# Optimization experiments

Measured on AMD Instinct MI355X. Metric: run time of the kernel, lower is better.

The kernel has to match this reference:

```python
import jax, jax.numpy as jnp
import numpy as np

B, T, NV, DEG, E = 64, 256, 20000, 8, 128
NSEG, NBUCKET = NV * DEG, 288
F_DIST, F_DIR, F_TT, HID = 50, 50, 50, 100
FEED = 2 * E + F_DIST + F_DIR  # 356


def setup_inputs() -> dict:
    key = jax.random.key(0)
    ks = jax.random.split(key, 32)
    s = 1.0 / np.sqrt(E)
    return {
        "xs_padded": jax.random.randint(ks[0], (B, T), 0, NV),
        "lengths": jax.random.randint(ks[1], (B,), 8, T + 1),
        "xs_actions": jax.random.randint(ks[2], (B, T - 1), 0, DEG),
        "destinations": jax.random.randint(ks[3], (B,), 0, NV),
        "adj_list": jax.random.randint(ks[4], (NV, DEG), 0, NV),
        "seg_ids": jax.random.randint(ks[5], (NV, DEG), 0, NSEG),
        "start_time": 42,
        "locations": jax.random.normal(ks[6], (NV, 2)),
        "time_dist_seg": jax.random.uniform(ks[7], (NSEG, NBUCKET)) * 10.0,
        "emb": jax.random.normal(ks[8], (NV + 2, E)) * 0.01,
        "Wq": jax.random.normal(ks[9], (E, E)) * s,
        "Wk": jax.random.normal(ks[10], (E, E)) * s,
        "Wv": jax.random.normal(ks[11], (E, E)) * s,
        "Wo": jax.random.normal(ks[12], (E, E)) * s,
        "dist_W": jax.random.normal(ks[13], (1, F_DIST)),
        "dist_b": jnp.zeros((F_DIST,)),
        "dir_W": jax.random.normal(ks[14], (2, F_DIR)) * 0.7,
        "dir_b": jnp.zeros((F_DIR,)),
        "tt_W": jax.random.normal(ks[15], (1, F_TT)),
        "tt_b": jnp.zeros((F_TT,)),
        "ob_W1": jax.random.normal(ks[16], (F_TT, F_TT // 2)) * (1.0 / np.sqrt(F_TT)),
        "ob_b1": jnp.zeros((F_TT // 2,)),
        "ob_W2": jax.random.normal(ks[17], (F_TT // 2, 1)) * (1.0 / np.sqrt(F_TT // 2)),
        "ob_b2": jnp.zeros((1,)),
        "om_W1": jax.random.normal(ks[18], (FEED, HID)) * (1.0 / np.sqrt(FEED)),
        "om_b1": jnp.zeros((HID,)),
        "om_W2": jax.random.normal(ks[19], (HID, HID // 2)) * (1.0 / np.sqrt(HID)),
        "om_b2": jnp.zeros((HID // 2,)),
        "om_W3": jax.random.normal(ks[20], (HID // 2, 1)) * (1.0 / np.sqrt(HID // 2)),
        "om_b3": jnp.zeros((1,)),
    }


def reference(xs_padded, lengths, xs_actions, destinations, adj_list, seg_ids,
              start_time, locations, time_dist_seg, emb, Wq, Wk, Wv, Wo,
              dist_W, dist_b, dir_W, dir_b, tt_W, tt_b,
              ob_W1, ob_b1, ob_W2, ob_b2,
              om_W1, om_b1, om_W2, om_b2, om_W3, om_b3):
    # --- embeddings + causal/padding-masked self-attention (flash_att) ---
    x_e = emb[xs_padded]                                       # [B,T,E]
    q, k, v = x_e @ Wq, x_e @ Wk, x_e @ Wv
    scores = jnp.einsum('bqe,bke->bqk', q, k) / jnp.sqrt(jnp.float32(E))
    causal = jnp.triu(jnp.ones((T, T), bool), 1)
    pad = jnp.arange(T)[None, :] >= lengths[:, None]           # key padding [B,T]
    scores = jnp.where(causal[None] | pad[:, None, :], -1e9, scores)
    hidden = jnp.einsum('bqk,bke->bqe', jax.nn.softmax(scores, axis=-1), v) @ Wo

    # --- irregular neighbor gather: route_neighbors only filled for t < len-1 ---
    valid_t = jnp.arange(T)[None, :] < (lengths - 1)[:, None]  # [B,T]
    rn = jnp.where(valid_t[:, :, None], adj_list[xs_padded], 0)  # [B,T,DEG]

    # --- distance to destination feature ---
    dest_c = locations[destinations][:, None, None, :]         # [B,1,1,2]
    nbr_c = locations[rn]                                      # [B,T,DEG,2]
    dist = jnp.abs(nbr_c - dest_c).sum(-1, keepdims=True) * 100.0
    dist_f = dist @ dist_W + dist_b

    # --- direction (unit vector) feature ---
    vec = nbr_c - locations[xs_padded][:, :, None, :]
    unit = vec / (jnp.linalg.norm(vec, axis=-1, keepdims=True) + 1e-8)
    dir_f = unit @ dir_W + dir_b

    # --- travel-time lookup + masked whitening ---
    nmask = rn != 0
    tt = time_dist_seg[seg_ids[xs_padded], start_time]         # [B,T,DEG]
    mf = nmask.astype(tt.dtype)
    cnt = mf.sum()
    mean = (tt * mf).sum() / cnt
    var = (((tt - mean) ** 2) * mf).sum() / (cnt - 1.0)        # unbiased, like torch.std
    tt = (tt - mean) / (jnp.sqrt(var) + 1e-6)
    tt_f = (tt[..., None] @ tt_W + tt_b) * mf[..., None]

    # --- fuse and score neighbors ---
    hid_e = jnp.broadcast_to(hidden[:, :, None, :], (B, T, DEG, E))
    dest_e = jnp.broadcast_to(emb[destinations][:, None, None, :], (B, T, DEG, E))
    feed = jnp.concatenate([hid_e, dist_f, dir_f, dest_e], axis=-1)  # [B,T,DEG,356]

    ob = (jax.nn.relu(tt_f @ ob_W1 + ob_b1) @ ob_W2 + ob_b2).squeeze(-1)
    h1 = jax.nn.relu(feed @ om_W1 + om_b1)
    h2 = jax.nn.relu(h1 @ om_W2 + om_b2)
    logits = (h2 @ om_W3 + om_b3).squeeze(-1) + ob             # [B,T,DEG]

    # --- per-route mean cross-entropy over valid transitions, summed over batch ---
    logp = jax.nn.log_softmax(logits[:, :T - 1], axis=-1)
    nll = -jnp.take_along_axis(logp, xs_actions[..., None], axis=-1).squeeze(-1)
    vmask = (jnp.arange(T - 1)[None, :] < (lengths - 1)[:, None]).astype(nll.dtype)
    per = (nll * vmask).sum(1) / (lengths - 1).astype(nll.dtype)
    return per.sum()
```

## Files before the change

### kernel.cpp

```cpp
#include <hip/hip_runtime.h>
#include <math.h>

#define BB 64
#define TT 256
#define DEG 8
#define EE 128
#define NBUCKET 288
#define HID 100
#define H2 50

constexpr size_t OFF_STATS   = 0;
constexpr size_t OFF_CDIST   = 4;
constexpr size_t OFF_CDIRX   = 104;
constexpr size_t OFF_CDIRY   = 204;
constexpr size_t OFF_BASE    = 304;
constexpr size_t OFF_V25     = 404;
constexpr size_t OFF_C25     = 429;
constexpr size_t OFF_OBZ     = 454;
constexpr size_t OFF_DESTPRE = 456;
constexpr size_t OFF_WF      = 6856;
constexpr size_t OFF_TT      = 32456;
constexpr size_t OFF_Q       = 163528;
constexpr size_t OFF_K       = OFF_Q + 16384 * 128;
constexpr size_t OFF_VP      = OFF_K + 16384 * 128;
constexpr size_t OFF_H1P     = OFF_VP + 16384 * 100;

__global__ void __launch_bounds__(256) k_setup(
    const int* destinations, const float* emb, const float* Wo,
    const float* dist_W, const float* dist_b, const float* dir_W, const float* dir_b,
    const float* tt_W, const float* tt_b, const float* ob_W1, const float* ob_b1,
    const float* ob_W2, const float* ob_b2, const float* om_W1, const float* om_b1,
    float* ws, float* out) {
    __shared__ float sh[EE];
    int blk = blockIdx.x;
    int j = threadIdx.x;
    if (blk == 0) {
        if (j < 4) ws[OFF_STATS + j] = 0.f;
        if (j == 0) out[0] = 0.f;
        if (j < HID) {
            float cd = 0.f, cx = 0.f, cy = 0.f, bs = om_b1[j];
            for (int f = 0; f < 50; f++) {
                float w1d = om_W1[(128 + f) * HID + j];
                float w1r = om_W1[(178 + f) * HID + j];
                cd += dist_W[f] * w1d;
                bs += dist_b[f] * w1d + dir_b[f] * w1r;
                cx += dir_W[f] * w1r;
                cy += dir_W[50 + f] * w1r;
            }
            ws[OFF_CDIST + j] = cd; ws[OFF_CDIRX + j] = cx;
            ws[OFF_CDIRY + j] = cy; ws[OFF_BASE + j] = bs;
        }
        if (j >= 128 && j < 153) {
            int jj = j - 128;
            float v = 0.f, c = ob_b1[jj];
            for (int i = 0; i < 50; i++) {
                v += tt_W[i] * ob_W1[i * 25 + jj];
                c += tt_b[i] * ob_W1[i * 25 + jj];
            }
            ws[OFF_V25 + jj] = v; ws[OFF_C25 + jj] = c;
        }
        if (j == 200) {
            float z = ob_b2[0];
            for (int i = 0; i < 25; i++) z += fmaxf(ob_b1[i], 0.f) * ob_W2[i];
            ws[OFF_OBZ] = z;
        }
    } else if (blk <= 64) {
        int b = blk - 1;
        if (j < EE) sh[j] = emb[(size_t)destinations[b] * EE + j];
        __syncthreads();
        if (j < HID) {
            float acc = 0.f;
            for (int i = 0; i < EE; i++) acc += sh[i] * om_W1[(228 + i) * HID + j];
            ws[OFF_DESTPRE + b * HID + j] = acc;
        }
    } else {
        int i = blk - 65;
        if (j < EE) sh[j] = Wo[i * EE + j];
        __syncthreads();
        if (j < HID) {
            float acc = 0.f;
            for (int jj = 0; jj < EE; jj++) acc += sh[jj] * om_W1[jj * HID + j];
            ws[OFF_WF + i * HID + j] = acc;
        }
    }
}

__global__ void __launch_bounds__(256) k_mid(
    const int* xs, const int* lengths, const int* adj, const int* seg,
    const int* stime, const float* tds, const float* emb,
    const float* Wq, const float* Wk, const float* Wv, float* ws) {
    __shared__ float smem[2 * 128 * 36 + 32];
    int blk = blockIdx.x;
    int tid = threadIdx.x;
    if (blk < 512) {
        float (*XT)[36]  = (float(*)[36])smem;
        float (*T1T)[36] = (float(*)[36])(smem + 128 * 36);
        int* vids = (int*)(smem + 2 * 128 * 36);
        int r0 = blk * 32;
        if (tid < 32) vids[tid] = xs[r0 + tid];
        __syncthreads();
        for (int c = 0; c < 16; c++) {
            int idx = c * 256 + tid;
            int r = idx >> 7, i = idx & 127;
            XT[i][r] = emb[(size_t)vids[r] * EE + i];
        }
        __syncthreads();
        int cg = tid & 31, rg = tid >> 5;
        const float* Wmats[2] = {Wq, Wk};
        float* Omats[2] = {ws + OFF_Q, ws + OFF_K};
        for (int mtx = 0; mtx < 2; mtx++) {
            const float* W = Wmats[mtx];
            float acc[4][4];
            #pragma unroll
            for (int a = 0; a < 4; a++)
                #pragma unroll
                for (int bb = 0; bb < 4; bb++) acc[a][bb] = 0.f;
            #pragma unroll 4
            for (int i = 0; i < EE; i++) {
                float4 av = *(const float4*)&XT[i][rg << 2];
                float4 wv = *(const float4*)&W[i * EE + (cg << 2)];
                acc[0][0] += av.x * wv.x; acc[0][1] += av.x * wv.y; acc[0][2] += av.x * wv.z; acc[0][3] += av.x * wv.w;
                acc[1][0] += av.y * wv.x; acc[1][1] += av.y * wv.y; acc[1][2] += av.y * wv.z; acc[1][3] += av.y * wv.w;
                acc[2][0] += av.z * wv.x; acc[2][1] += av.z * wv.y; acc[2][2] += av.z * wv.z; acc[2][3] += av.z * wv.w;
                acc[3][0] += av.w * wv.x; acc[3][1] += av.w * wv.y; acc[3][2] += av.w * wv.z; acc[3][3] += av.w * wv.w;
            }
            float* O = Omats[mtx];
            #pragma unroll
            for (int jj = 0; jj < 4; jj++)
                *(float4*)&O[(size_t)(r0 + (rg << 2) + jj) * EE + (cg << 2)] =
                    make_float4(acc[jj][0], acc[jj][1], acc[jj][2], acc[jj][3]);
        }
        {
            float acc[4][4];
            #pragma unroll
            for (int a = 0; a < 4; a++)
                #pragma unroll
                for (int bb = 0; bb < 4; bb++) acc[a][bb] = 0.f;
            #pragma unroll 4
            for (int i = 0; i < EE; i++) {
                float4 av = *(const float4*)&XT[i][rg << 2];
                float4 wv = *(const float4*)&Wv[i * EE + (cg << 2)];
                acc[0][0] += av.x * wv.x; acc[0][1] += av.x * wv.y; acc[0][2] += av.x * wv.z; acc[0][3] += av.x * wv.w;
                acc[1][0] += av.y * wv.x; acc[1][1] += av.y * wv.y; acc[1][2] += av.y * wv.z; acc[1][3] += av.y * wv.w;
                acc[2][0] += av.z * wv.x; acc[2][1] += av.z * wv.y; acc[2][2] += av.z * wv.z; acc[2][3] += av.z * wv.w;
                acc[3][0] += av.w * wv.x; acc[3][1] += av.w * wv.y; acc[3][2] += av.w * wv.z; acc[3][3] += av.w * wv.w;
            }
            #pragma unroll
            for (int jj = 0; jj < 4; jj++)
                #pragma unroll
                for (int ii = 0; ii < 4; ii++)
                    T1T[(cg << 2) + ii][(rg << 2) + jj] = acc[jj][ii];
        }
        __syncthreads();
        if (cg < 25) {
            const float* WF = ws + OFF_WF;
            float acc[4][4];
            #pragma unroll
            for (int a = 0; a < 4; a++)
                #pragma unroll
                for (int bb = 0; bb < 4; bb++) acc[a][bb] = 0.f;
            #pragma unroll 4
            for (int i = 0; i < EE; i++) {
                float4 av = *(const float4*)&T1T[i][rg << 2];
                float4 wv = *(const float4*)&WF[i * HID + (cg << 2)];
                acc[0][0] += av.x * wv.x; acc[0][1] += av.x * wv.y; acc[0][2] += av.x * wv.z; acc[0][3] += av.x * wv.w;
                acc[1][0] += av.y * wv.x; acc[1][1] += av.y * wv.y; acc[1][2] += av.y * wv.z; acc[1][3] += av.y * wv.w;
                acc[2][0] += av.z * wv.x; acc[2][1] += av.z * wv.y; acc[2][2] += av.z * wv.z; acc[2][3] += av.z * wv.w;
                acc[3][0] += av.w * wv.x; acc[3][1] += av.w * wv.y; acc[3][2] += av.w * wv.z; acc[3][3] += av.w * wv.w;
            }
            float* VP = ws + OFF_VP;
            #pragma unroll
            for (int jj = 0; jj < 4; jj++)
                *(float4*)&VP[(size_t)(r0 + (rg << 2) + jj) * HID + (cg << 2)] =
                    make_float4(acc[jj][0], acc[jj][1], acc[jj][2], acc[jj][3]);
        }
    } else {
        float* rs = smem; float* rq = smem + 256; float* rc = smem + 512;
        int st = *stime;
        float lsum = 0.f, lsq = 0.f, lcnt = 0.f;
        int total = BB * TT * DEG;
        for (int idx = (blk - 512) * 256 + tid; idx < total; idx += 256 * 256) {
            int d = idx & 7;
            int bt = idx >> 3;
            int t = bt & 255;
            int b = bt >> 8;
            int len = lengths[b];
            if (t >= len - 1) continue;
            int v = xs[bt];
            int sg = seg[v * DEG + d];
            float tt = tds[(size_t)sg * NBUCKET + st];
            ws[OFF_TT + idx] = tt;
            int a = adj[v * DEG + d];
            if (a != 0) { lsum += tt; lsq += tt * tt; lcnt += 1.f; }
        }
        rs[tid] = lsum; rq[tid] = lsq; rc[tid] = lcnt;
        __syncthreads();
        for (int s = 128; s > 0; s >>= 1) {
            if (tid < s) { rs[tid] += rs[tid + s]; rq[tid] += rq[tid + s]; rc[tid] += rc[tid + s]; }
            __syncthreads();
        }
        if (tid == 0) {
            atomicAdd(&ws[OFF_STATS + 0], rs[0]);
            atomicAdd(&ws[OFF_STATS + 1], rq[0]);
            atomicAdd(&ws[OFF_STATS + 2], rc[0]);
        }
    }
}

__global__ void __launch_bounds__(256) k_attn(const int* lengths, float* ws) {
    int b = blockIdx.x >> 4;
    int tile = blockIdx.x & 15;
    int t0 = tile << 4;
    int len = lengths[b];
    if (t0 >= len - 1) return;
    int nk = t0 + 16;
    int nm = nk >> 4;
    __shared__ float Qs[16][132];
    __shared__ float S[16][260];
    __shared__ float KV[32 * 136];
    int tid = threadIdx.x;
    const float* Q  = ws + OFF_Q;
    const float* K  = ws + OFF_K;
    const float* VP = ws + OFF_VP;
    {
        const float* Qg = Q + ((size_t)(b * TT + t0)) * EE;
        for (int idx = tid; idx < 512; idx += 256) {
            int r = idx >> 5, c4 = (idx & 31) << 2;
            *(float4*)&Qs[r][c4] = *(const float4*)&Qg[r * EE + c4];
        }
    }
    int q = tid >> 4, li = tid & 15;
    int tq = t0 + q;
    float sreg[16];
    #pragma unroll
    for (int m = 0; m < 16; m++) sreg[m] = -1e30f;
    float (*Ks)[136] = (float(*)[136])KV;
    int ktend = ((nk + 31) >> 5) << 5;
    for (int kt = 0; kt < ktend; kt += 32) {
        __syncthreads();
        const float* Kg = K + ((size_t)(b * TT + kt)) * EE;
        for (int idx = tid; idx < 1024; idx += 256) {
            int r = idx >> 5, c4 = (idx & 31) << 2;
            *(float4*)&Ks[r][c4] = *(const float4*)&Kg[r * EE + c4];
        }
        __syncthreads();
        int k0 = kt + li, k1 = kt + li + 16;
        float s0 = 0.f, s1 = 0.f;
        const float4* q4  = (const float4*)Qs[q];
        const float4* k4a = (const float4*)Ks[li];
        const float4* k4b = (const float4*)Ks[li + 16];
        #pragma unroll 8
        for (int i = 0; i < 32; i++) {
            float4 a = q4[i];
            float4 x = k4a[i];
            float4 y = k4b[i];
            s0 += a.x * x.x + a.y * x.y + a.z * x.z + a.w * x.w;
            s1 += a.x * y.x + a.y * y.y + a.z * y.z + a.w * y.w;
        }
        int m0 = kt >> 4;
        if (k0 < nk && k0 <= tq) sreg[m0]     = s0 * 0.08838834764831845f;
        if (k1 < nk && k1 <= tq) sreg[m0 + 1] = s1 * 0.08838834764831845f;
    }
    float mx = -1e30f;
    for (int m = 0; m < nm; m++) mx = fmaxf(mx, sreg[m]);
    #pragma unroll
    for (int o = 1; o < 16; o <<= 1) mx = fmaxf(mx, __shfl_xor(mx, o, 16));
    float lsum = 0.f;
    for (int m = 0; m < nm; m++) { float p = __expf(sreg[m] - mx); sreg[m] = p; lsum += p; }
    #pragma unroll
    for (int o = 1; o < 16; o <<= 1) lsum += __shfl_xor(lsum, o, 16);
    float inv = 1.f / lsum;
    for (int m = 0; m < nm; m++) S[q][li + (m << 4)] = sreg[m];
    float acc[7];
    #pragma unroll
    for (int j = 0; j < 7; j++) acc[j] = 0.f;
    float (*Vs)[104] = (float(*)[104])KV;
    for (int vt = 0; vt < nk; vt += 32) {
        __syncthreads();
        const float* Vg = VP + ((size_t)(b * TT + vt)) * HID;
        for (int idx = tid; idx < 800; idx += 256) {
            int r = idx / 25, c4 = (idx - r * 25) << 2;
            *(float4*)&Vs[r][c4] = *(const float4*)&Vg[r * HID + c4];
        }
        __syncthreads();
        int kmax = nk - vt; if (kmax > 32) kmax = 32;
        for (int k = 0; k < kmax; k++) {
            float p = S[q][vt + k];
            #pragma unroll
            for (int j = 0; j < 7; j++) {
                int c = li + (j << 4);
                if (c < HID) acc[j] += p * Vs[k][c];
            }
        }
    }
    if (tq < len - 1) {
        float* H = ws + OFF_H1P + (size_t)(b * TT + tq) * HID;
        const float* BASEv = ws + OFF_BASE;
        const float* DP = ws + OFF_DESTPRE + b * HID;
        #pragma unroll
        for (int j = 0; j < 7; j++) {
            int c = li + (j << 4);
            if (c < HID) H[c] = acc[j] * inv + BASEv[c] + DP[c];
        }
    }
}

__global__ void __launch_bounds__(256) k_final(
    const int* xs, const int* lengths, const int* xs_actions, const int* destinations,
    const int* adj, const float* locations,
    const float* om_W2, const float* om_b2, const float* om_W3, const float* om_b3,
    const float* ob_W2, const float* ob_b2,
    const float* ws, float* out)
{
    __shared__ float W2T[H2][104];
    __shared__ float h1s[4][DEG][104];
    __shared__ float nlls[4];
    int tid = threadIdx.x;
    for (int idx = tid; idx < HID * H2; idx += 256) {
        int mm = idx / H2, n = idx - mm * H2;
        W2T[n][mm] = om_W2[idx];
    }
    if (tid < 4) nlls[tid] = 0.f;
    int w = tid >> 6, lane = tid & 63;
    int r = lane >> 3, li = lane & 7;
    float sum = ws[OFF_STATS], sq = ws[OFF_STATS + 1], cnt = ws[OFF_STATS + 2];
    float mean = sum / cnt;
    float var = (sq - cnt * mean * mean) / (cnt - 1.f);
    float sdinv = 1.f / (sqrtf(var) + 1e-6f);
    __syncthreads();
    for (int it = 0; it < 4; it++) {
        int pi = blockIdx.x * 16 + it * 4 + w;
        int b = pi / (TT - 1), t = pi - b * (TT - 1);
        int len = lengths[b];
        bool valid = (t < len - 1);
        int bt = b * TT + t;
        if (valid) {
            float distv = 0.f, uxv = 0.f, uyv = 0.f, obv = 0.f;
            if (lane < 8) {
                int v = xs[bt];
                int a = adj[v * DEG + lane];
                float nbx = locations[2 * a], nby = locations[2 * a + 1];
                int dst = destinations[b];
                float dxl = locations[2 * dst], dyl = locations[2 * dst + 1];
                float cxl = locations[2 * v], cyl = locations[2 * v + 1];
                distv = (fabsf(nbx - dxl) + fabsf(nby - dyl)) * 100.f;
                float vx = nbx - cxl, vy = nby - cyl;
                float nrm = sqrtf(vx * vx + vy * vy) + 1e-8f;
                uxv = vx / nrm; uyv = vy / nrm;
                float ttn = (ws[OFF_TT + (size_t)bt * 8 + lane] - mean) * sdinv;
                float obp = 0.f;
                for (int j = 0; j < 25; j++)
                    obp += fmaxf(ttn * ws[OFF_V25 + j] + ws[OFF_C25 + j], 0.f) * ob_W2[j];
                obv = (a != 0) ? (obp + ob_b2[0]) : ws[OFF_OBZ];
            }
            distv = __shfl(distv, r, 64);
            uxv   = __shfl(uxv, r, 64);
            uyv   = __shfl(uyv, r, 64);
            obv   = __shfl(obv, r, 64);
            const float* H = ws + OFF_H1P + (size_t)bt * HID;
            for (int mm = li; mm < HID; mm += 8) {
                float pre = H[mm] + distv * ws[OFF_CDIST + mm]
                          + uxv * ws[OFF_CDIRX + mm] + uyv * ws[OFF_CDIRY + mm];
                h1s[w][r][mm] = fmaxf(pre, 0.f);
            }
            float acc[7] = {0.f, 0.f, 0.f, 0.f, 0.f, 0.f, 0.f};
            const float4* hv4 = (const float4*)h1s[w][r];
            for (int ks = 0; ks < 25; ks++) {
                float4 h = hv4[ks];
                #pragma unroll
                for (int j = 0; j < 7; j++) {
                    int n = li + 8 * j;
                    if (n < H2) {
                        float4 wv = *(const float4*)&W2T[n][ks << 2];
                        acc[j] += h.x * wv.x + h.y * wv.y + h.z * wv.z + h.w * wv.w;
                    }
                }
            }
            float part = 0.f;
            #pragma unroll
            for (int j = 0; j < 7; j++) {
                int n = li + 8 * j;
                if (n < H2) part += fmaxf(acc[j] + om_b2[n], 0.f) * om_W3[n];
            }
            part += __shfl_xor(part, 1, 8);
            part += __shfl_xor(part, 2, 8);
            part += __shfl_xor(part, 4, 8);
            float logit = part + om_b3[0] + obv;
            float lgv[8];
            float mx = -1e30f;
            #pragma unroll
            for (int d = 0; d < 8; d++) {
                lgv[d] = __shfl(logit, d << 3, 64);
                mx = fmaxf(mx, lgv[d]);
            }
            if (lane == 0) {
                int act = xs_actions[b * (TT - 1) + t];
                float se = 0.f, sel = 0.f;
                #pragma unroll
                for (int d = 0; d < 8; d++) {
                    se += __expf(lgv[d] - mx);
                    if (d == act) sel = lgv[d];
                }
                float nll = mx + __logf(se) - sel;
                nlls[w] += nll / (float)(len - 1);
            }
        }
    }
    __syncthreads();
    if (tid == 0) {
        atomicAdd(out, nlls[0] + nlls[1] + nlls[2] + nlls[3]);
    }
}

extern "C" void kernel_launch(void* const* d_in, const int* in_sizes, int n_in,
                              void* d_out, int out_size, void* d_ws, size_t ws_size,
                              hipStream_t stream) {
    const int* xs_padded    = (const int*)d_in[0];
    const int* lengths      = (const int*)d_in[1];
    const int* xs_actions   = (const int*)d_in[2];
    const int* destinations = (const int*)d_in[3];
    const int* adj_list     = (const int*)d_in[4];
    const int* seg_ids      = (const int*)d_in[5];
    const int* start_time   = (const int*)d_in[6];
    const float* locations  = (const float*)d_in[7];
    const float* tds        = (const float*)d_in[8];
    const float* emb        = (const float*)d_in[9];
    const float* Wq         = (const float*)d_in[10];
    const float* Wk         = (const float*)d_in[11];
    const float* Wv         = (const float*)d_in[12];
    const float* Wo         = (const float*)d_in[13];
    const float* dist_W     = (const float*)d_in[14];
    const float* dist_b     = (const float*)d_in[15];
    const float* dir_W      = (const float*)d_in[16];
    const float* dir_b      = (const float*)d_in[17];
    const float* tt_W       = (const float*)d_in[18];
    const float* tt_b       = (const float*)d_in[19];
    const float* ob_W1      = (const float*)d_in[20];
    const float* ob_b1      = (const float*)d_in[21];
    const float* ob_W2      = (const float*)d_in[22];
    const float* ob_b2      = (const float*)d_in[23];
    const float* om_W1      = (const float*)d_in[24];
    const float* om_b1      = (const float*)d_in[25];
    const float* om_W2      = (const float*)d_in[26];
    const float* om_b2      = (const float*)d_in[27];
    const float* om_W3      = (const float*)d_in[28];
    const float* om_b3      = (const float*)d_in[29];
    float* ws  = (float*)d_ws;
    float* out = (float*)d_out;

    k_setup<<<193, 256, 0, stream>>>(destinations, emb, Wo, dist_W, dist_b,
                                     dir_W, dir_b, tt_W, tt_b, ob_W1, ob_b1,
                                     ob_W2, ob_b2, om_W1, om_b1, ws, out);
    k_mid<<<768, 256, 0, stream>>>(xs_padded, lengths, adj_list, seg_ids,
                                   start_time, tds, emb, Wq, Wk, Wv, ws);
    k_attn<<<BB * 16, 256, 0, stream>>>(lengths, ws);
    k_final<<<1020, 256, 0, stream>>>(
        xs_padded, lengths, xs_actions, destinations, adj_list, locations,
        om_W2, om_b2, om_W3, om_b3, ob_W2, ob_b2, ws, out);
}
```

Before: 483.9 us.

## Fuse attention and final MLP scoring into one kernel via shared memory

Merges the attention kernel and the final scoring kernel so the per-position hidden pre-activation stays in shared memory rather than being written to and read back from a global workspace buffer. The second MLP layer is reorganised as a register-tiled 2x8 outer-product over a transposed h1 tile, computing all 8 neighbors for 8 queries per pass. This removes one launch and a global round trip, but it adds shared-memory reuse across phases and puts the MLP work on the attention blocks' schedule and occupancy.

Result: faster. 471.5 us (-2.6%).

```diff
diff --git a/kernel.cpp b/kernel.cpp
--- a/kernel.cpp
+++ b/kernel.cpp
@@ -23,7 +23,6 @@
 constexpr size_t OFF_Q       = 163528;
 constexpr size_t OFF_K       = OFF_Q + 16384 * 128;
 constexpr size_t OFF_VP      = OFF_K + 16384 * 128;
-constexpr size_t OFF_H1P     = OFF_VP + 16384 * 100;
 
 __global__ void __launch_bounds__(256) k_setup(
     const int* destinations, const float* emb, const float* Wo,
@@ -207,18 +206,26 @@
     }
 }
 
-__global__ void __launch_bounds__(256) k_attn(const int* lengths, float* ws) {
+__global__ void __launch_bounds__(256) k_attnfinal(
+    const int* lengths, const int* xs, const int* xs_actions,
+    const int* destinations, const int* adj, const float* locations,
+    const float* om_W2, const float* om_b2, const float* om_W3, const float* om_b3,
+    const float* ob_W2, const float* ob_b2,
+    float* ws, float* out) {
     int b = blockIdx.x >> 4;
     int tile = blockIdx.x & 15;
     int t0 = tile << 4;
     int len = lengths[b];
     if (t0 >= len - 1) return;
+    int nqv = len - 1 - t0; if (nqv > 16) nqv = 16;
     int nk = t0 + 16;
     int nm = nk >> 4;
-    __shared__ float Qs[16][132];
-    __shared__ float S[16][260];
-    __shared__ float KV[32 * 136];
+    __shared__ float smem[17696];
+    float (*S)[260]  = (float(*)[260])smem;
+    float (*Qs)[132] = (float(*)[132])(smem + 4160);
+    float* KV = smem + 6272;
     int tid = threadIdx.x;
+    if (tid < 16) smem[17680 + tid] = 0.f;
     const float* Q  = ws + OFF_Q;
     const float* K  = ws + OFF_K;
     const float* VP = ws + OFF_VP;
@@ -293,122 +300,152 @@
             }
         }
     }
-    if (tq < len - 1) {
-        float* H = ws + OFF_H1P + (size_t)(b * TT + tq) * HID;
+    __syncthreads();
+    {
         const float* BASEv = ws + OFF_BASE;
         const float* DP = ws + OFF_DESTPRE + b * HID;
         #pragma unroll
         for (int j = 0; j < 7; j++) {
             int c = li + (j << 4);
-            if (c < HID) H[c] = acc[j] * inv + BASEv[c] + DP[c];
-        }
-    }
-}
-
-__global__ void __launch_bounds__(256) k_final(
-    const int* xs, const int* lengths, const int* xs_actions, const int* destinations,
-    const int* adj, const float* locations,
-    const float* om_W2, const float* om_b2, const float* om_W3, const float* om_b3,
-    const float* ob_W2, const float* ob_b2,
-    const float* ws, float* out)
-{
-    __shared__ float W2T[H2][104];
-    __shared__ float h1s[4][DEG][104];
-    __shared__ float nlls[4];
-    int tid = threadIdx.x;
-    for (int idx = tid; idx < HID * H2; idx += 256) {
-        int mm = idx / H2, n = idx - mm * H2;
-        W2T[n][mm] = om_W2[idx];
-    }
-    if (tid < 4) nlls[tid] = 0.f;
-    int w = tid >> 6, lane = tid & 63;
-    int r = lane >> 3, li = lane & 7;
-    float sum = ws[OFF_STATS], sq = ws[OFF_STATS + 1], cnt = ws[OFF_STATS + 2];
-    float mean = sum / cnt;
-    float var = (sq - cnt * mean * mean) / (cnt - 1.f);
-    float sdinv = 1.f / (sqrtf(var) + 1e-6f);
+            if (c < HID) S[q][c] = acc[j] * inv + BASEv[c] + DP[c];
+        }
+    }
+    float (*W2s)[64] = (float(*)[64])(smem + 4160);
+    for (int idx = tid; idx < 6400; idx += 256) {
+        int mm = idx >> 6, n = idx & 63;
+        W2s[mm][n] = (n < H2) ? om_W2[mm * H2 + n] : 0.f;
+    }
+    float smean, sdinv;
+    {
+        float sum = ws[OFF_STATS], sq = ws[OFF_STATS + 1], cnt = ws[OFF_STATS + 2];
+        smean = sum / cnt;
+        float var = (sq - cnt * smean * smean) / (cnt - 1.f);
+        sdinv = 1.f / (sqrtf(var) + 1e-6f);
+    }
+    float (*h1T)[68] = (float(*)[68])(smem + 10560);
+    float* distR = smem + 17360;
+    float* uxR   = smem + 17424;
+    float* uyR   = smem + 17488;
+    float* obR   = smem + 17552;
+    float* lgS   = smem + 17616;
+    float* nllS  = smem + 17680;
+    int cg = tid & 7, rg = tid >> 3;
+    float b2v[8], w3v[8];
+    #pragma unroll
+    for (int k = 0; k < 8; k++) {
+        int n = (cg << 3) + k;
+        b2v[k] = (n < H2) ? om_b2[n] : 0.f;
+        w3v[k] = (n < H2) ? om_W3[n] : 0.f;
+    }
+    float ob2s = ob_b2[0];
+    float obz = ws[OFF_OBZ];
     __syncthreads();
-    for (int it = 0; it < 4; it++) {
-        int pi = blockIdx.x * 16 + it * 4 + w;
-        int b = pi / (TT - 1), t = pi - b * (TT - 1);
-        int len = lengths[b];
-        bool valid = (t < len - 1);
-        int bt = b * TT + t;
-        if (valid) {
-            float distv = 0.f, uxv = 0.f, uyv = 0.f, obv = 0.f;
-            if (lane < 8) {
-                int v = xs[bt];
-                int a = adj[v * DEG + lane];
-                float nbx = locations[2 * a], nby = locations[2 * a + 1];
-                int dst = destinations[b];
-                float dxl = locations[2 * dst], dyl = locations[2 * dst + 1];
-                float cxl = locations[2 * v], cyl = locations[2 * v + 1];
-                distv = (fabsf(nbx - dxl) + fabsf(nby - dyl)) * 100.f;
-                float vx = nbx - cxl, vy = nby - cyl;
-                float nrm = sqrtf(vx * vx + vy * vy) + 1e-8f;
-                uxv = vx / nrm; uyv = vy / nrm;
-                float ttn = (ws[OFF_TT + (size_t)bt * 8 + lane] - mean) * sdinv;
-                float obp = 0.f;
-                for (int j = 0; j < 25; j++)
-                    obp += fmaxf(ttn * ws[OFF_V25 + j] + ws[OFF_C25 + j], 0.f) * ob_W2[j];
-                obv = (a != 0) ? (obp + ob_b2[0]) : ws[OFF_OBZ];
-            }
-            distv = __shfl(distv, r, 64);
-            uxv   = __shfl(uxv, r, 64);
-            uyv   = __shfl(uyv, r, 64);
-            obv   = __shfl(obv, r, 64);
-            const float* H = ws + OFF_H1P + (size_t)bt * HID;
-            for (int mm = li; mm < HID; mm += 8) {
-                float pre = H[mm] + distv * ws[OFF_CDIST + mm]
-                          + uxv * ws[OFF_CDIRX + mm] + uyv * ws[OFF_CDIRY + mm];
-                h1s[w][r][mm] = fmaxf(pre, 0.f);
-            }
-            float acc[7] = {0.f, 0.f, 0.f, 0.f, 0.f, 0.f, 0.f};
-            const float4* hv4 = (const float4*)h1s[w][r];
-            for (int ks = 0; ks < 25; ks++) {
-                float4 h = hv4[ks];
-                #pragma unroll
-                for (int j = 0; j < 7; j++) {
-                    int n = li + 8 * j;
-                    if (n < H2) {
-                        float4 wv = *(const float4*)&W2T[n][ks << 2];
-                        acc[j] += h.x * wv.x + h.y * wv.y + h.z * wv.z + h.w * wv.w;
-                    }
+    for (int qh = 0; qh < 2; qh++) {
+        if (tid < 64) {
+            int ql = tid >> 3, d = tid & 7;
+            int qa = (qh << 3) + ql;
+            int t = t0 + qa;
+            int bt = b * TT + t;
+            int v = xs[bt];
+            int a = adj[v * DEG + d];
+            float nbx = locations[2 * a], nby = locations[2 * a + 1];
+            int dst = destinations[b];
+            float dxl = locations[2 * dst], dyl = locations[2 * dst + 1];
+            float cxl = locations[2 * v], cyl = locations[2 * v + 1];
+            distR[tid] = (fabsf(nbx - dxl) + fabsf(nby - dyl)) * 100.f;
+            float vx = nbx - cxl, vy = nby - cyl;
+            float nrm = sqrtf(vx * vx + vy * vy) + 1e-8f;
+            uxR[tid] = vx / nrm; uyR[tid] = vy / nrm;
+            float ttn = (ws[OFF_TT + (size_t)bt * 8 + d] - smean) * sdinv;
+            float obp = 0.f;
+            for (int j = 0; j < 25; j++)
+                obp += fmaxf(ttn * ws[OFF_V25 + j] + ws[OFF_C25 + j], 0.f) * ob_W2[j];
+            obR[tid] = (a != 0) ? (obp + ob2s) : obz;
+        }
+        __syncthreads();
+        {
+            int r = tid & 63, mq = tid >> 6;
+            int qa = (qh << 3) + (r >> 3);
+            float dv = distR[r], ux = uxR[r], uy = uyR[r];
+            const float* CD = ws + OFF_CDIST;
+            const float* CX = ws + OFF_CDIRX;
+            const float* CY = ws + OFF_CDIRY;
+            const float* Hq = S[qa];
+            int m0 = mq * 25;
+            #pragma unroll 5
+            for (int mi = 0; mi < 25; mi++) {
+                int m = m0 + mi;
+                float pre = Hq[m] + dv * CD[m] + ux * CX[m] + uy * CY[m];
+                h1T[m][r] = fmaxf(pre, 0.f);
+            }
+        }
+        __syncthreads();
+        {
+            float facc[2][8];
+            #pragma unroll
+            for (int jr = 0; jr < 2; jr++)
+                #pragma unroll
+                for (int k = 0; k < 8; k++) facc[jr][k] = 0.f;
+            int r0 = rg << 1, n0 = cg << 3;
+            #pragma unroll 4
+            for (int m = 0; m < HID; m++) {
+                float2 hv = *(const float2*)&h1T[m][r0];
+                float4 w0 = *(const float4*)&W2s[m][n0];
+                float4 w1 = *(const float4*)&W2s[m][n0 + 4];
+                facc[0][0] += hv.x * w0.x; facc[0][1] += hv.x * w0.y;
+                facc[0][2] += hv.x * w0.z; facc[0][3] += hv.x * w0.w;
+                facc[0][4] += hv.x * w1.x; facc[0][5] += hv.x * w1.y;
+                facc[0][6] += hv.x * w1.z; facc[0][7] += hv.x * w1.w;
+                facc[1][0] += hv.y * w0.x; facc[1][1] += hv.y * w0.y;
+                facc[1][2] += hv.y * w0.z; facc[1][3] += hv.y * w0.w;
+                facc[1][4] += hv.y * w1.x; facc[1][5] += hv.y * w1.y;
+                facc[1][6] += hv.y * w1.z; facc[1][7] += hv.y * w1.w;
+            }
+            #pragma unroll
+            for (int jr = 0; jr < 2; jr++) {
+                float part = 0.f;
+                #pragma unroll
+                for (int k = 0; k < 8; k++)
+                    part += fmaxf(facc[jr][k] + b2v[k], 0.f) * w3v[k];
+                part += __shfl_xor(part, 1, 64);
+                part += __shfl_xor(part, 2, 64);
+                part += __shfl_xor(part, 4, 64);
+                if (cg == 0) {
+                    int row = r0 + jr;
+                    lgS[row] = part + om_b3[0] + obR[row];
                 }
             }
-            float part = 0.f;
-            #pragma unroll
-            for (int j = 0; j < 7; j++) {
-                int n = li + 8 * j;
-                if (n < H2) part += fmaxf(acc[j] + om_b2[n], 0.f) * om_W3[n];
-            }
-            part += __shfl_xor(part, 1, 8);
-            part += __shfl_xor(part, 2, 8);
-            part += __shfl_xor(part, 4, 8);
-            float logit = part + om_b3[0] + obv;
-            float lgv[8];
-            float mx = -1e30f;
-            #pragma unroll
-            for (int d = 0; d < 8; d++) {
-                lgv[d] = __shfl(logit, d << 3, 64);
-                mx = fmaxf(mx, lgv[d]);
-            }
-            if (lane == 0) {
+        }
+        __syncthreads();
+        if (tid < 8) {
+            int qa = (qh << 3) + tid;
+            if (qa < nqv) {
+                int t = t0 + qa;
+                float lg[8];
+                float mxl = -1e30f;
+                #pragma unroll
+                for (int d = 0; d < 8; d++) {
+                    lg[d] = lgS[(tid << 3) + d];
+                    mxl = fmaxf(mxl, lg[d]);
+                }
                 int act = xs_actions[b * (TT - 1) + t];
                 float se = 0.f, sel = 0.f;
                 #pragma unroll
                 for (int d = 0; d < 8; d++) {
-                    se += __expf(lgv[d] - mx);
-                    if (d == act) sel = lgv[d];
+                    se += __expf(lg[d] - mxl);
+                    if (d == act) sel = lg[d];
                 }
-                float nll = mx + __logf(se) - sel;
-                nlls[w] += nll / (float)(len - 1);
-            }
-        }
-    }
-    __syncthreads();
+                float nll = mxl + __logf(se) - sel;
+                nllS[qa] = nll / (float)(len - 1);
+            }
+        }
+        __syncthreads();
+    }
     if (tid == 0) {
-        atomicAdd(out, nlls[0] + nlls[1] + nlls[2] + nlls[3]);
+        float s = 0.f;
+        #pragma unroll
+        for (int i = 0; i < 16; i++) s += nllS[i];
+        atomicAdd(out, s);
     }
 }
 
@@ -453,8 +490,7 @@
                                      ob_W2, ob_b2, om_W1, om_b1, ws, out);
     k_mid<<<768, 256, 0, stream>>>(xs_padded, lengths, adj_list, seg_ids,
                                    start_time, tds, emb, Wq, Wk, Wv, ws);
-    k_attn<<<BB * 16, 256, 0, stream>>>(lengths, ws);
-    k_final<<<1020, 256, 0, stream>>>(
-        xs_padded, lengths, xs_actions, destinations, adj_list, locations,
+    k_attnfinal<<<BB * 16, 256, 0, stream>>>(
+        lengths, xs_padded, xs_actions, destinations, adj_list, locations,
         om_W2, om_b2, om_W3, om_b3, ob_W2, ob_b2, ws, out);
 }
```
